# Performance work log

Measured on AMD Instinct MI355X. Metric: run time of the kernel, lower is better.

## Reference

```python
import jax, jax.numpy as jnp
import numpy as np

BATCH, IN_F, OUT_F = 8192, 4096, 4096


def setup_inputs() -> dict:
    key = jax.random.key(0)
    kx, kw = jax.random.split(key)
    x = jax.random.normal(kx, (BATCH, IN_F), dtype=jnp.float32)
    # weights binarized to {-1, +1} as in __init__ (uniform(-1,1) then sign)
    W = jnp.where(jax.random.normal(kw, (OUT_F, IN_F)) > 0, 1.0, -1.0).astype(jnp.float32)
    return {"x": x, "W": W}


def reference(x, W):
    # forward: input thresholded to {0,1} (x>0 -> 1, else 0), then x_bin @ W^T, no bias
    x_bin = (x > 0).astype(x.dtype)
    return jnp.matmul(x_bin, W.T)  # [batch, out_features]
```

## Files before the change

kernel.cpp:

```cpp
#include <hip/hip_runtime.h>
#include <stdint.h>

typedef __attribute__((ext_vector_type(4)))  int   v4i;
typedef __attribute__((ext_vector_type(8)))  int   v8i;
typedef __attribute__((ext_vector_type(16))) float v16f;

#define BATCH 8192
#define KDIM  4096
#define NOUT  4096
#define KB    (KDIM / 2)
#define BK_B  128
#define NT    (KDIM / 256)

__global__ __launch_bounds__(256) void pack_x4(const float* __restrict__ x,
                                               uint32_t* __restrict__ xb) {
    int t = blockIdx.x * 256 + threadIdx.x;
    const float4* p = (const float4*)x + (size_t)t * 2;
    float4 f0 = p[0];
    float4 f1 = p[1];
    uint32_t b = (f0.x > 0.f ? 0x2u        : 0u)
               | (f0.y > 0.f ? 0x20u       : 0u)
               | (f0.z > 0.f ? 0x200u      : 0u)
               | (f0.w > 0.f ? 0x2000u     : 0u)
               | (f1.x > 0.f ? 0x20000u    : 0u)
               | (f1.y > 0.f ? 0x200000u   : 0u)
               | (f1.z > 0.f ? 0x2000000u  : 0u)
               | (f1.w > 0.f ? 0x20000000u : 0u);
    xb[t] = b;
}

__global__ __launch_bounds__(256) void pack_wf(const float* __restrict__ w,
                                               uint32_t* __restrict__ wf) {
    int u = blockIdx.x * 256 + threadIdx.x;
    int lane = u & 63;
    int T    = (u >> 6) & 63;
    int g    = u >> 12;
    const float* src = w + (size_t)(g * 32 + (lane & 31)) * KDIM
                         + T * 64 + (lane >> 5) * 32;
    uint32_t wd[4];
    #pragma unroll
    for (int i = 0; i < 4; ++i) {
        float4 f0 = ((const float4*)src)[i * 2];
        float4 f1 = ((const float4*)src)[i * 2 + 1];
        wd[i] = (f0.x > 0.f ? 0x2u        : 0xAu)
              | (f0.y > 0.f ? 0x20u       : 0xA0u)
              | (f0.z > 0.f ? 0x200u      : 0xA00u)
              | (f0.w > 0.f ? 0x2000u     : 0xA000u)
              | (f1.x > 0.f ? 0x20000u    : 0xA0000u)
              | (f1.y > 0.f ? 0x200000u   : 0xA00000u)
              | (f1.z > 0.f ? 0x2000000u  : 0xA000000u)
              | (f1.w > 0.f ? 0x20000000u : 0xA0000000u);
    }
    ((uint4*)wf)[u] = make_uint4(wd[0], wd[1], wd[2], wd[3]);
}

__global__ __launch_bounds__(512, 2) void bin_gemm4(const uint8_t* __restrict__ A,
                                                    const uint8_t* __restrict__ Bf,
                                                    float* __restrict__ C) {
    __shared__ __align__(16) uint8_t sm[65536];

    const int tid  = threadIdx.x;
    const int w    = tid >> 6;
    const int lane = tid & 63;
    const int l31  = lane & 31;
    const int kc   = lane >> 5;
    const int rsw  = lane & 7;

    const int Mbase = blockIdx.y * 256;
    const int Nbase = blockIdx.x * 256;
    const int wm = (w >> 2) * 128;
    const int wn = (w & 3) * 64;

    const int srow = w * 32 + (lane >> 3);
    const int swz  = ((lane & 7) ^ ((lane >> 3) & 7)) * 16;
    const uint8_t* pA = A + (size_t)(Mbase + srow) * KB + swz;

    const uint8_t* pBf = Bf + (size_t)((Nbase + wn) >> 5) * 65536 + (size_t)lane * 16;

    v16f acc[4][2] = {};

    #pragma unroll
    for (int L = 0; L < 4; ++L)
        __builtin_amdgcn_global_load_lds(
            (__attribute__((address_space(1))) void*)(pA + (size_t)(L * 8) * KB),
            (__attribute__((address_space(3))) void*)(sm + (w * 32 + L * 8) * 128),
            16, 0, 0);
    __syncthreads();

    for (int t = 0; t < NT; ++t) {
        v4i bfr[2][4];
        #pragma unroll
        for (int nb = 0; nb < 2; ++nb)
            #pragma unroll
            for (int ks = 0; ks < 4; ++ks)
                bfr[nb][ks] = *(const v4i*)(pBf + (size_t)(nb * 64 + t * 4 + ks) * 1024);

        if (t + 1 < NT) {
            const int nbuf = (t + 1) & 1;
            const int kof  = (t + 1) * BK_B;
            #pragma unroll
            for (int L = 0; L < 4; ++L)
                __builtin_amdgcn_global_load_lds(
                    (__attribute__((address_space(1))) void*)(pA + (size_t)(L * 8) * KB + kof),
                    (__attribute__((address_space(3))) void*)(sm + nbuf * 32768 + (w * 32 + L * 8) * 128),
                    16, 0, 0);
        }

        const uint8_t* sA = sm + (t & 1) * 32768;
        #pragma unroll
        for (int ks = 0; ks < 4; ++ks) {
            const int slot = ((ks * 2 + kc) ^ rsw) * 16;
            v8i b8[2];
            #pragma unroll
            for (int nb = 0; nb < 2; ++nb)
                b8[nb] = (v8i){bfr[nb][ks][0], bfr[nb][ks][1],
                               bfr[nb][ks][2], bfr[nb][ks][3], 0, 0, 0, 0};
            #pragma unroll
            for (int mb = 0; mb < 4; ++mb) {
                v4i af = *(const v4i*)(sA + (wm + mb * 32 + l31) * 128 + slot);
                v8i a8 = {af[0], af[1], af[2], af[3], 0, 0, 0, 0};
                #pragma unroll
                for (int nb = 0; nb < 2; ++nb)
                    acc[mb][nb] = __builtin_amdgcn_mfma_scale_f32_32x32x64_f8f6f4(
                        a8, b8[nb], acc[mb][nb], 4, 4,
                        0, 0x7F7F7F7F, 0, 0x7F7F7F7F);
            }
        }

        __syncthreads();
    }

    float* Cp = C + (size_t)(Mbase + wm + 4 * kc) * NOUT + (Nbase + wn + l31);
    #pragma unroll
    for (int mb = 0; mb < 4; ++mb)
        #pragma unroll
        for (int nb = 0; nb < 2; ++nb)
            #pragma unroll
            for (int r = 0; r < 16; ++r)
                Cp[(size_t)(mb * 32 + (r & 3) + 8 * (r >> 2)) * NOUT + nb * 32]
                    = acc[mb][nb][r];
}

extern "C" void kernel_launch(void* const* d_in, const int* in_sizes, int n_in,
                              void* d_out, int out_size, void* d_ws, size_t ws_size,
                              hipStream_t stream) {
    const float* x = (const float*)d_in[0];
    const float* W = (const float*)d_in[1];
    float* out = (float*)d_out;

    uint8_t* xb = (uint8_t*)d_ws;
    uint8_t* wf = (uint8_t*)d_ws + (size_t)BATCH * KDIM / 2;

    pack_x4<<<(BATCH * (size_t)KDIM / 8) / 256, 256, 0, stream>>>(x, (uint32_t*)xb);
    pack_wf<<<(128 * 64 * 64) / 256, 256, 0, stream>>>(W, (uint32_t*)wf);

    dim3 grid(NOUT / 256, BATCH / 256);
    bin_gemm4<<<grid, 512, 0, stream>>>(xb, wf, out);
}
```

Before: 333.3 us.

## Pre-pack A into MFMA fragment layout and load both operands directly to registers

The activation pack kernel now writes x into the same fragment-major layout already used for W. The GEMM reads A fragments straight from global memory into registers, so the LDS staging, async global-to-LDS copies and per-tile barriers are gone. The launch becomes a 1D grid with a block swizzle that groups tiles for cache locality. In exchange, A is no longer shared through LDS across the four N-warps of a block, so redundant global/L2 traffic rises and load latency is hidden only by occupancy and the compiler, with no explicit double buffering.

New measurement: 423.6 us. 27.1% more time.

```diff
diff --git a/kernel.cpp b/kernel.cpp
--- a/kernel.cpp
+++ b/kernel.cpp
@@ -8,25 +8,31 @@
 #define BATCH 8192
 #define KDIM  4096
 #define NOUT  4096
-#define KB    (KDIM / 2)
-#define BK_B  128
 #define NT    (KDIM / 256)
 
-__global__ __launch_bounds__(256) void pack_x4(const float* __restrict__ x,
-                                               uint32_t* __restrict__ xb) {
-    int t = blockIdx.x * 256 + threadIdx.x;
-    const float4* p = (const float4*)x + (size_t)t * 2;
-    float4 f0 = p[0];
-    float4 f1 = p[1];
-    uint32_t b = (f0.x > 0.f ? 0x2u        : 0u)
-               | (f0.y > 0.f ? 0x20u       : 0u)
-               | (f0.z > 0.f ? 0x200u      : 0u)
-               | (f0.w > 0.f ? 0x2000u     : 0u)
-               | (f1.x > 0.f ? 0x20000u    : 0u)
-               | (f1.y > 0.f ? 0x200000u   : 0u)
-               | (f1.z > 0.f ? 0x2000000u  : 0u)
-               | (f1.w > 0.f ? 0x20000000u : 0u);
-    xb[t] = b;
+__global__ __launch_bounds__(256) void pack_af(const float* __restrict__ x,
+                                               uint32_t* __restrict__ af) {
+    int u = blockIdx.x * 256 + threadIdx.x;
+    int lane = u & 63;
+    int T    = (u >> 6) & 63;
+    int g    = u >> 12;
+    const float* src = x + (size_t)(g * 32 + (lane & 31)) * KDIM
+                         + T * 64 + (lane >> 5) * 32;
+    uint32_t wd[4];
+    #pragma unroll
+    for (int i = 0; i < 4; ++i) {
+        float4 f0 = ((const float4*)src)[i * 2];
+        float4 f1 = ((const float4*)src)[i * 2 + 1];
+        wd[i] = (f0.x > 0.f ? 0x2u        : 0u)
+              | (f0.y > 0.f ? 0x20u       : 0u)
+              | (f0.z > 0.f ? 0x200u      : 0u)
+              | (f0.w > 0.f ? 0x2000u     : 0u)
+              | (f1.x > 0.f ? 0x20000u    : 0u)
+              | (f1.y > 0.f ? 0x200000u   : 0u)
+              | (f1.z > 0.f ? 0x2000000u  : 0u)
+              | (f1.w > 0.f ? 0x20000000u : 0u);
+    }
+    ((uint4*)af)[u] = make_uint4(wd[0], wd[1], wd[2], wd[3]);
 }
 
 __global__ __launch_bounds__(256) void pack_wf(const float* __restrict__ w,
@@ -54,62 +60,46 @@
     ((uint4*)wf)[u] = make_uint4(wd[0], wd[1], wd[2], wd[3]);
 }
 
-__global__ __launch_bounds__(512, 2) void bin_gemm4(const uint8_t* __restrict__ A,
-                                                    const uint8_t* __restrict__ Bf,
-                                                    float* __restrict__ C) {
-    __shared__ __align__(16) uint8_t sm[65536];
-
+__global__ __launch_bounds__(512, 2) void bin_gemm_rs(const uint8_t* __restrict__ Af,
+                                                      const uint8_t* __restrict__ Bf,
+                                                      float* __restrict__ C) {
     const int tid  = threadIdx.x;
     const int w    = tid >> 6;
     const int lane = tid & 63;
     const int l31  = lane & 31;
     const int kc   = lane >> 5;
-    const int rsw  = lane & 7;
 
-    const int Mbase = blockIdx.y * 256;
-    const int Nbase = blockIdx.x * 256;
+    const int bid = blockIdx.x;
+    const int swz = (bid & 7) * 64 + (bid >> 3);
+    const int by  = swz >> 4;
+    const int bx  = swz & 15;
+
+    const int Mbase = by * 256;
+    const int Nbase = bx * 256;
     const int wm = (w >> 2) * 128;
     const int wn = (w & 3) * 64;
 
-    const int srow = w * 32 + (lane >> 3);
-    const int swz  = ((lane & 7) ^ ((lane >> 3) & 7)) * 16;
-    const uint8_t* pA = A + (size_t)(Mbase + srow) * KB + swz;
-
-    const uint8_t* pBf = Bf + (size_t)((Nbase + wn) >> 5) * 65536 + (size_t)lane * 16;
+    const uint8_t* pA = Af + (size_t)((Mbase + wm) >> 5) * 65536 + (size_t)lane * 16;
+    const uint8_t* pB = Bf + (size_t)((Nbase + wn) >> 5) * 65536 + (size_t)lane * 16;
 
     v16f acc[4][2] = {};
 
-    #pragma unroll
-    for (int L = 0; L < 4; ++L)
-        __builtin_amdgcn_global_load_lds(
-            (__attribute__((address_space(1))) void*)(pA + (size_t)(L * 8) * KB),
-            (__attribute__((address_space(3))) void*)(sm + (w * 32 + L * 8) * 128),
-            16, 0, 0);
-    __syncthreads();
+    for (int t = 0; t < NT; ++t) {
+        const size_t tof = (size_t)t * 4096;
 
-    for (int t = 0; t < NT; ++t) {
-        v4i bfr[2][4];
+        v4i afr[4][4], bfr[2][4];
         #pragma unroll
-        for (int nb = 0; nb < 2; ++nb)
+        for (int ks = 0; ks < 4; ++ks) {
             #pragma unroll
-            for (int ks = 0; ks < 4; ++ks)
-                bfr[nb][ks] = *(const v4i*)(pBf + (size_t)(nb * 64 + t * 4 + ks) * 1024);
-
-        if (t + 1 < NT) {
-            const int nbuf = (t + 1) & 1;
-            const int kof  = (t + 1) * BK_B;
+            for (int mb = 0; mb < 4; ++mb)
+                afr[mb][ks] = *(const v4i*)(pA + tof + (size_t)(mb * 64 + ks) * 1024);
             #pragma unroll
-            for (int L = 0; L < 4; ++L)
-                __builtin_amdgcn_global_load_lds(
-                    (__attribute__((address_space(1))) void*)(pA + (size_t)(L * 8) * KB + kof),
-                    (__attribute__((address_space(3))) void*)(sm + nbuf * 32768 + (w * 32 + L * 8) * 128),
-                    16, 0, 0);
+            for (int nb = 0; nb < 2; ++nb)
+                bfr[nb][ks] = *(const v4i*)(pB + tof + (size_t)(nb * 64 + ks) * 1024);
         }
 
-        const uint8_t* sA = sm + (t & 1) * 32768;
         #pragma unroll
         for (int ks = 0; ks < 4; ++ks) {
-            const int slot = ((ks * 2 + kc) ^ rsw) * 16;
             v8i b8[2];
             #pragma unroll
             for (int nb = 0; nb < 2; ++nb)
@@ -117,8 +107,8 @@
                                bfr[nb][ks][2], bfr[nb][ks][3], 0, 0, 0, 0};
             #pragma unroll
             for (int mb = 0; mb < 4; ++mb) {
-                v4i af = *(const v4i*)(sA + (wm + mb * 32 + l31) * 128 + slot);
-                v8i a8 = {af[0], af[1], af[2], af[3], 0, 0, 0, 0};
+                v8i a8 = {afr[mb][ks][0], afr[mb][ks][1],
+                          afr[mb][ks][2], afr[mb][ks][3], 0, 0, 0, 0};
                 #pragma unroll
                 for (int nb = 0; nb < 2; ++nb)
                     acc[mb][nb] = __builtin_amdgcn_mfma_scale_f32_32x32x64_f8f6f4(
@@ -126,8 +116,6 @@
                         0, 0x7F7F7F7F, 0, 0x7F7F7F7F);
             }
         }
-
-        __syncthreads();
     }
 
     float* Cp = C + (size_t)(Mbase + wm + 4 * kc) * NOUT + (Nbase + wn + l31);
@@ -148,12 +136,11 @@
     const float* W = (const float*)d_in[1];
     float* out = (float*)d_out;
 
-    uint8_t* xb = (uint8_t*)d_ws;
+    uint8_t* af = (uint8_t*)d_ws;
     uint8_t* wf = (uint8_t*)d_ws + (size_t)BATCH * KDIM / 2;
 
-    pack_x4<<<(BATCH * (size_t)KDIM / 8) / 256, 256, 0, stream>>>(x, (uint32_t*)xb);
+    pack_af<<<(256 * 64 * 64) / 256, 256, 0, stream>>>(x, (uint32_t*)af);
     pack_wf<<<(128 * 64 * 64) / 256, 256, 0, stream>>>(W, (uint32_t*)wf);
 
-    dim3 grid(NOUT / 256, BATCH / 256);
-    bin_gemm4<<<grid, 512, 0, stream>>>(xb, wf, out);
+    bin_gemm_rs<<<512, 512, 0, stream>>>(af, wf, out);
 }
```
